# Kernel optimization log

Measured on AMD Instinct MI355X. Metric: run time of the kernel, lower is better.

The kernel has to match this reference:

```python
import jax, jax.numpy as jnp
import numpy as np

EMBED_DIM = 1024
BATCH = 4
SEQ = 2048


def setup_inputs() -> dict:
    key = jax.random.key(0)
    ks = jax.random.split(key, 9)
    D = EMBED_DIM
    s = 1.0 / np.sqrt(D)
    inputs = jax.random.normal(ks[0], (BATCH, SEQ, D), dtype=jnp.float32)
    rotation_params = jax.random.normal(ks[1], (D, D), dtype=jnp.float32) * s
    entangle_params = jax.random.normal(ks[2], (D, D), dtype=jnp.float32) * s
    Wq = jax.random.normal(ks[3], (D, D), dtype=jnp.float32) * s
    bq = jax.random.normal(ks[4], (D,), dtype=jnp.float32) * 0.01
    Wk = jax.random.normal(ks[5], (D, D), dtype=jnp.float32) * s
    bk = jax.random.normal(ks[6], (D,), dtype=jnp.float32) * 0.01
    Wv = jax.random.normal(ks[7], (D, D), dtype=jnp.float32) * s
    bv = jax.random.normal(ks[8], (D,), dtype=jnp.float32) * 0.01
    # causal mask: True = masked out (matches torch masked_fill semantics)
    mask = jnp.triu(jnp.ones((SEQ, SEQ), dtype=bool), k=1)
    return {"inputs": inputs, "rotation_params": rotation_params,
            "entangle_params": entangle_params, "Wq": Wq, "bq": bq,
            "Wk": Wk, "bk": bk, "Wv": Wv, "bv": bv, "mask": mask}


def reference(inputs, rotation_params, entangle_params, Wq, bq, Wk, bk, Wv, bv, mask):
    D = inputs.shape[-1]
    # q = Linear(x) @ R^T ; k = Linear(x) @ E^T ; v = Linear(x)
    q = (jnp.einsum('bsd,ed->bse', inputs, Wq) + bq) @ rotation_params.T
    k = (jnp.einsum('bsd,ed->bse', inputs, Wk) + bk) @ entangle_params.T
    v = jnp.einsum('bsd,ed->bse', inputs, Wv) + bv
    scores = jnp.einsum('bqd,bkd->bqk', q, k) / jnp.sqrt(jnp.float32(D))
    scores = jnp.where(mask, jnp.float32(-jnp.inf), scores)
    probs = jax.nn.softmax(scores, axis=-1)  # dropout=0.0 -> identity
    return jnp.einsum('bqk,bkd->bqd', probs, v)
```

## Files before the change

kernel.cpp:

```cpp
#include <hip/hip_runtime.h>
#include <hip/hip_bf16.h>
#include <stdint.h>
#include <math.h>

#define DD 1024
#define SS 2048
#define BB 4

typedef __bf16 bf16;
typedef __bf16 bf16x8 __attribute__((ext_vector_type(8)));
typedef __bf16 bf16x4 __attribute__((ext_vector_type(4)));
typedef float f32x4 __attribute__((ext_vector_type(4)));

__device__ __forceinline__ void gload_lds16(const bf16* g, bf16* l) {
  __builtin_amdgcn_global_load_lds(
      (const __attribute__((address_space(1))) void*)g,
      (__attribute__((address_space(3))) void*)l, 16, 0, 0);
}

__global__ __launch_bounds__(256) void prep_all(
    const float* __restrict__ x, const float* __restrict__ R,
    const float* __restrict__ E, const float* __restrict__ Wv,
    const float* __restrict__ Wq, const float* __restrict__ Wk,
    const float* __restrict__ bq, const float* __restrict__ bk,
    const float* __restrict__ bv, bf16* __restrict__ xb,
    bf16* __restrict__ Rb, bf16* __restrict__ Eb, bf16* __restrict__ Wvb,
    bf16* __restrict__ WqT, bf16* __restrict__ WkT, float* __restrict__ bias,
    float* __restrict__ rowsums) {
  int bid = blockIdx.x;
  int t = threadIdx.x;
  if (bid < 11264) {
    const float* src;
    bf16* dst;
    int base;
    if (bid < 8192) { src = x; dst = xb; base = bid; }
    else if (bid < 9216) { src = R; dst = Rb; base = bid - 8192; }
    else if (bid < 10240) { src = E; dst = Eb; base = bid - 9216; }
    else { src = Wv; dst = Wvb; base = bid - 10240; }
    int i = (base * 256 + t) * 4;
    float4 v = *(const float4*)(src + i);
    bf16x4 o;
    o.x = (bf16)v.x; o.y = (bf16)v.y; o.z = (bf16)v.z; o.w = (bf16)v.w;
    *(bf16x4*)(dst + i) = o;
  } else if (bid < 13312) {
    int r2 = bid - 11264;
    const float* src = (r2 >= 1024) ? Wk : Wq;
    bf16* dst = (r2 >= 1024) ? WkT : WqT;
    int rem = r2 & 1023;
    int bx = rem & 31, by = rem >> 5;
    __shared__ float tile[32][33];
    int tx = t & 31, ty = t >> 5;
    int xcol = bx * 32 + tx;
    int y0 = by * 32;
    for (int r = ty; r < 32; r += 8)
      tile[r][tx] = src[(y0 + r) * DD + xcol];
    __syncthreads();
    int dx = by * 32 + tx;
    int dy0 = bx * 32;
    for (int r = ty; r < 32; r += 8)
      dst[(dy0 + r) * DD + dx] = (bf16)tile[tx][r];
  } else if (bid < 16384) {
    int e = bid - 13312;
    if (e >= 2048) { if (t == 0) bias[e] = bv[e - 2048]; return; }
    const float* M = (e < 1024) ? R : E;
    const float* bb = (e < 1024) ? bq : bk;
    int row = e & 1023;
    float s = 0.f;
    for (int f = t; f < DD; f += 256) s += M[row * DD + f] * bb[f];
    for (int o = 32; o >= 1; o >>= 1) s += __shfl_xor(s, o, 64);
    __shared__ float red[4];
    if ((t & 63) == 0) red[t >> 6] = s;
    __syncthreads();
    if (t == 0) bias[e] = red[0] + red[1] + red[2] + red[3];
  } else {
    int idx = (bid - 16384) * 256 + t;
    rowsums[idx] = 0.f;
  }
}

#define QSTGA(pa, kt)                                                        \
  gload_lds16(A + (long)(w * 16 + srow) * DD + (kt) * 32 + scg,              \
              As + (pa) * 4096 + w * 512)
#define QSTGB(pb, h, kt)                                                     \
  gload_lds16(B + (long)((h) * 128 + w * 16 + srow) * DD + (kt) * 32 + scg,  \
              Bs + (pb) * 8192 + (h) * 4096 + w * 512)

#define QTILE(pa, pb, pa1, pb2, kA, kB, DOA, DOB, WAITN)                     \
  {                                                                          \
    bf16x8 af[4], bfr[4];                                                    \
    _Pragma("unroll") for (int i_ = 0; i_ < 4; i_++)                         \
        af[i_] = *(const bf16x8*)(a_base + (pa) * 4096 + i_ * 512);          \
    _Pragma("unroll") for (int j_ = 0; j_ < 4; j_++)                         \
        bfr[j_] = *(const bf16x8*)(b_base + (pb) * 8192 + j_ * 512);         \
    if (DOA) { QSTGA(pa1, kA); }                                             \
    if (DOB) { QSTGB(pb2, 0, kB); QSTGB(pb2, 1, kB); }                       \
    __builtin_amdgcn_s_barrier();                                            \
    asm volatile("s_waitcnt lgkmcnt(0)" ::: "memory");                       \
    __builtin_amdgcn_sched_barrier(0);                                       \
    __builtin_amdgcn_s_setprio(1);                                           \
    _Pragma("unroll") for (int i_ = 0; i_ < 4; i_++)                         \
        _Pragma("unroll") for (int j_ = 0; j_ < 4; j_++) acc[i_][j_] =       \
        __builtin_amdgcn_mfma_f32_16x16x32_bf16(af[i_], bfr[j_],             \
                                                acc[i_][j_], 0, 0, 0);       \
    __builtin_amdgcn_s_setprio(0);                                           \
    __builtin_amdgcn_sched_barrier(0);                                       \
    if ((WAITN) == 2) asm volatile("s_waitcnt vmcnt(2)" ::: "memory");       \
    if ((WAITN) == 0) asm volatile("s_waitcnt vmcnt(0)" ::: "memory");       \
    __builtin_amdgcn_s_barrier();                                            \
    __builtin_amdgcn_sched_barrier(0);                                       \
  }

__global__ __launch_bounds__(512, 4) void gemm_qkv(
    const bf16* __restrict__ Ag, const bf16* __restrict__ Bg,
    bf16* __restrict__ Cg, const float* __restrict__ bias,
    bf16* __restrict__ vTp) {
  __shared__ __align__(16) bf16 smem[32768];
  bf16* As = smem;
  bf16* Bs = smem + 8192;

  int id = (int)blockIdx.y * 12 + (int)blockIdx.x;
  int wg = (id & 7) * 96 + (id >> 3);
  int ck = wg / 96, r96 = wg % 96;
  int bx = (ck & 3) * 3 + r96 % 3;
  int by = (ck >> 2) * 32 + r96 / 3;
  long m0 = (long)by * 128, n0 = (long)bx * 256;
  const bf16* A = Ag + m0 * DD;
  const bf16* B = Bg + n0 * DD;

  int t = threadIdx.x;
  int w = t >> 6, l = t & 63;
  int wm = w >> 2, wn = w & 3;
  int ln = l & 15, quad = l >> 4;

  int srow = l >> 2;
  int scg = ((l & 3) ^ ((l >> 3) & 3)) * 8;
  int rdslot = (quad ^ ((ln >> 1) & 3)) * 8;
  const bf16* a_base = As + (wm * 64 + ln) * 32 + rdslot;
  const bf16* b_base = Bs + (wn * 64 + ln) * 32 + rdslot;

  f32x4 acc[4][4];
#pragma unroll
  for (int i = 0; i < 4; i++)
#pragma unroll
    for (int j = 0; j < 4; j++) acc[i][j] = f32x4{0.f, 0.f, 0.f, 0.f};

  QSTGA(0, 0);
  QSTGB(0, 0, 0); QSTGB(0, 1, 0);
  QSTGB(1, 0, 1); QSTGB(1, 1, 1);
  asm volatile("s_waitcnt vmcnt(2)" ::: "memory");
  __builtin_amdgcn_s_barrier();
  __builtin_amdgcn_sched_barrier(0);

#pragma unroll 1
  for (int t6 = 0; t6 < 30; t6 += 6) {
    QTILE(0, 0, 1, 2, t6 + 1, t6 + 2, 1, 1, 2)
    QTILE(1, 1, 0, 0, t6 + 2, t6 + 3, 1, 1, 2)
    QTILE(0, 2, 1, 1, t6 + 3, t6 + 4, 1, 1, 2)
    QTILE(1, 0, 0, 2, t6 + 4, t6 + 5, 1, 1, 2)
    QTILE(0, 1, 1, 0, t6 + 5, t6 + 6, 1, 1, 2)
    QTILE(1, 2, 0, 1, t6 + 6, t6 + 7, 1, 1, 2)
  }
  QTILE(0, 0, 1, 0, 31, 0, 1, 0, 0)
  QTILE(1, 1, 0, 0, 0, 0, 0, 0, -1)

  __syncthreads();

  if (n0 < 2048) {
    bf16* C = Cg + m0 * 3072 + n0;
#pragma unroll
    for (int i = 0; i < 4; i++) {
      int rb = wm * 64 + i * 16 + quad * 4;
#pragma unroll
      for (int j = 0; j < 4; j++) {
        int col = wn * 64 + j * 16 + ln;
        float bv_ = bias[n0 + col];
#pragma unroll
        for (int r = 0; r < 4; r++)
          C[(long)(rb + r) * 3072 + col] = (bf16)(acc[i][j][r] + bv_);
      }
    }
  } else {
    int d0 = (int)n0 - 2048;
    int b = (int)(m0 >> 11);
    int s0 = (int)(m0 & 2047);
#pragma unroll
    for (int i = 0; i < 4; i++) {
      int sl = wm * 64 + i * 16 + quad * 4;
#pragma unroll
      for (int j = 0; j < 4; j++) {
        int d = wn * 64 + j * 16 + ln;
        float bv_ = bias[n0 + d];
#pragma unroll
        for (int r = 0; r < 4; r++)
          smem[d * 128 + ((sl + r) ^ ((d & 7) << 3))] =
              (bf16)(acc[i][j][r] + bv_);
      }
    }
    __syncthreads();
    int d = t >> 1, sh = t & 1;
    bf16* dst = vTp + (long)b * DD * SS + (long)(d0 + d) * SS + s0 + sh * 64;
#pragma unroll
    for (int c = 0; c < 8; ++c) {
      int sc = (sh * 64 + c * 8) ^ ((d & 7) << 3);
      *(bf16x8*)(dst + c * 8) = *(const bf16x8*)(smem + d * 128 + sc);
    }
  }
}

template <int MODE>
__global__ __launch_bounds__(256, 4)
void gemm_bt(const bf16* __restrict__ Ag, long lda, long sAb,
             const bf16* __restrict__ Bg, long ldb, long sBb,
             void* __restrict__ Cg, long ldc, long sCb,
             const float* __restrict__ bias, float scale, int K,
             bf16* __restrict__ vTp, float* __restrict__ rowsums) {
  __shared__ __align__(16) bf16 smem[16384];
  bf16* As = smem;
  bf16* Bs = smem + 8192;

  int bx = blockIdx.x, by = blockIdx.y, bz = blockIdx.z;
  if (MODE == 0 || MODE == 1) {
    int nx = (int)gridDim.x;
    int nwg = nx * (int)gridDim.y;
    int id = by * nx + bx;
    int xcd = id & 7, rest = id >> 3;
    int q8 = nwg >> 3, r8 = nwg & 7;
    int wg = (xcd < r8 ? xcd * (q8 + 1) : r8 * (q8 + 1) + (xcd - r8) * q8)
             + rest;
    bx = wg % nx;
    by = wg / nx;
  }
  if (MODE == 1) {
    int q = bx;
    by = (int)((sqrtf(8.f * q + 1.f) - 1.f) * 0.5f);
    while ((by + 1) * (by + 2) / 2 <= q) by++;
    while (by * (by + 1) / 2 > q) by--;
    bx = q - by * (by + 1) / 2;
  }
  if (MODE == 2) by = 15 - by;
  long m0 = (long)by * 128, n0 = (long)bx * 128;
  const bf16* A = Ag + (long)bz * sAb + m0 * lda;
  const bf16* Bp = Bg + (long)bz * sBb + n0 * ldb;

  int t = threadIdx.x;
  int w = t >> 6, l = t & 63;
  int lr = l >> 2;
  int lc = (((l & 3) ^ (lr & 3)) * 8);
  int quad = l >> 4, ln = l & 15;
  int wm = w >> 1, wn = w & 1;
  int rdoff = ((quad ^ (ln & 3)) * 8);

  int Keff = (MODE == 2) ? (by + 1) * 128 : K;

  f32x4 acc[4][4];
#pragma unroll
  for (int i = 0; i < 4; i++)
#pragma unroll
    for (int j = 0; j < 4; j++) acc[i][j] = f32x4{0.f, 0.f, 0.f, 0.f};

  const bf16* a_base = As + (wm * 64 + ln) * 32 + rdoff;
  const bf16* b_base = Bs + (wn * 64 + ln) * 32 + rdoff;
  long arow0 = (long)(w * 16 + lr);

#define STG(p, kc0)                                                         \
  {                                                                         \
    int kc = (kc0) + lc;                                                    \
    gload_lds16(A + arow0 * lda + kc, As + (p) * 4096 + w * 512);           \
    gload_lds16(A + (arow0 + 64) * lda + kc,                                \
                As + (p) * 4096 + 2048 + w * 512);                          \
    gload_lds16(Bp + arow0 * ldb + kc, Bs + (p) * 4096 + w * 512);          \
    gload_lds16(Bp + (arow0 + 64) * ldb + kc,                               \
                Bs + (p) * 4096 + 2048 + w * 512);                          \
  }

  STG(0, 0);
  int cur = 0;
  for (int k = 0; k < Keff; k += 32) {
    asm volatile("s_waitcnt vmcnt(0)" ::: "memory");
    __builtin_amdgcn_s_barrier();
    __builtin_amdgcn_sched_barrier(0);
    if (k + 32 < Keff) STG(cur ^ 1, k + 32);
    bf16x8 af[4], bfr[4];
#pragma unroll
    for (int i = 0; i < 4; i++) {
      af[i] = *(const bf16x8*)(a_base + cur * 4096 + i * 512);
      bfr[i] = *(const bf16x8*)(b_base + cur * 4096 + i * 512);
    }
#pragma unroll
    for (int i = 0; i < 4; i++)
#pragma unroll
      for (int j = 0; j < 4; j++)
        acc[i][j] = __builtin_amdgcn_mfma_f32_16x16x32_bf16(
            af[i], bfr[j], acc[i][j], 0, 0, 0);
    cur ^= 1;
  }
#undef STG
  __syncthreads();

  if (MODE == 0) {
    bf16* C = (bf16*)Cg + (long)bz * sCb + m0 * ldc + n0;
#pragma unroll
    for (int i = 0; i < 4; i++) {
      int rb = wm * 64 + i * 16 + quad * 4;
#pragma unroll
      for (int j = 0; j < 4; j++) {
        int col = wn * 64 + j * 16 + ln;
        float bv_ = bias ? bias[n0 + col] : 0.f;
#pragma unroll
        for (int r = 0; r < 4; r++)
          C[(long)(rb + r) * ldc + col] = (bf16)(acc[i][j][r] + bv_);
      }
    }
  } else if (MODE == 1) {
#pragma unroll
    for (int i = 0; i < 4; i++) {
      int rb = wm * 64 + i * 16 + quad * 4;
#pragma unroll
      for (int j = 0; j < 4; j++) {
        int col = wn * 64 + j * 16 + ln;
#pragma unroll
        for (int r = 0; r < 4; r++) {
          int row = rb + r;
          float p = 0.f;
          if (n0 + col <= m0 + row) p = __expf(acc[i][j][r] * scale);
          smem[row * 128 + (col ^ ((row & 15) << 3))] = (bf16)p;
        }
      }
    }
    __syncthreads();
    int row = t >> 1, h = t & 1;
    bf16* P = (bf16*)Cg + (long)bz * sCb + (m0 + row) * ldc + n0;
    float rsum = 0.f;
#pragma unroll
    for (int jj = 0; jj < 8; jj++) {
      int p8 = h * 8 + jj;
      int slot = p8 ^ (row & 15);
      bf16x8 v = *(const bf16x8*)(smem + row * 128 + slot * 8);
#pragma unroll
      for (int e = 0; e < 8; e++) rsum += (float)v[e];
      *(bf16x8*)(P + p8 * 8) = v;
    }
    atomicAdd(&rowsums[(long)bz * SS + m0 + row], rsum);
  } else {
    float* C = (float*)Cg + (long)bz * sCb + m0 * ldc + n0;
    const float* rs = rowsums + (long)bz * SS + m0;
#pragma unroll
    for (int i = 0; i < 4; i++) {
      int rb = wm * 64 + i * 16 + quad * 4;
      float inv[4];
#pragma unroll
      for (int r = 0; r < 4; r++) inv[r] = 1.f / rs[rb + r];
#pragma unroll
      for (int j = 0; j < 4; j++) {
        int col = wn * 64 + j * 16 + ln;
#pragma unroll
        for (int r = 0; r < 4; r++)
          C[(long)(rb + r) * ldc + col] = acc[i][j][r] * inv[r];
      }
    }
  }
}

extern "C" void kernel_launch(void* const* d_in, const int* in_sizes, int n_in,
                              void* d_out, int out_size, void* d_ws,
                              size_t ws_size, hipStream_t stream) {
  const float* x = (const float*)d_in[0];
  const float* R = (const float*)d_in[1];
  const float* E = (const float*)d_in[2];
  const float* Wq = (const float*)d_in[3];
  const float* bq = (const float*)d_in[4];
  const float* Wk = (const float*)d_in[5];
  const float* bk = (const float*)d_in[6];
  const float* Wv = (const float*)d_in[7];
  const float* bv = (const float*)d_in[8];
  float* out = (float*)d_out;

  char* ws = (char*)d_ws;
  bf16* qkv = (bf16*)ws;
  bf16* vT = (bf16*)(ws + 50331648);
  bf16* probs = (bf16*)(ws + 67108864);
  float* rowsums = (float*)(ws + 100663296);
  char* sr = ws + 101711872;
  bf16* xb = (bf16*)sr;
  bf16* Rb = (bf16*)(sr + 16777216);
  bf16* Eb = Rb + 1024 * 1024;
  bf16* WqT = (bf16*)(sr + 20971520);
  bf16* WkT = WqT + 1024 * 1024;
  bf16* wcat = (bf16*)(sr + 25165824);
  float* bias = (float*)(sr + 31457280);

  prep_all<<<16416, 256, 0, stream>>>(x, R, E, Wv, Wq, Wk, bq, bk, bv, xb, Rb,
                                      Eb, wcat + 2048 * DD, WqT, WkT, bias,
                                      rowsums);

  gemm_bt<0><<<dim3(8, 8, 2), 256, 0, stream>>>(
      Rb, DD, 1024 * 1024, WqT, DD, 1024 * 1024, wcat, DD, 1024 * 1024,
      nullptr, 1.f, DD, nullptr, nullptr);

  gemm_qkv<<<dim3(12, 64, 1), 512, 0, stream>>>(xb, wcat, qkv, bias, vT);

  gemm_bt<1><<<dim3(136, 1, BB), 256, 0, stream>>>(
      qkv, 3072, (long)SS * 3072, qkv + 1024, 3072, (long)SS * 3072, probs,
      SS, (long)SS * SS, nullptr, 0.03125f, DD, nullptr, rowsums);

  gemm_bt<2><<<dim3(8, 16, BB), 256, 0, stream>>>(
      probs, SS, (long)SS * SS, vT, SS, (long)DD * SS, out,
      DD, (long)SS * DD, nullptr, 1.f, SS, nullptr, rowsums);
}
```

Baseline: 293.2 us.

## Replace causal scores GEMM with 128x256-tile, 512-thread pipelined kernel

The QK^T scores stage moves out of the generic 128x128 gemm_bt MODE 1 path into a dedicated scores256 kernel. It reuses the gemm_qkv triple-buffered LDS pipeline with 512 threads and 128x256 tiles, and enumerates only causal tiles through a square-root mapping combined with XCD-aware ordering. Its epilogue applies exp and the causal mask, writes P through swizzled LDS, and reduces row sums with shuffles before the atomic add. The larger tiles should give more data reuse per block and fewer launched blocks, at the cost of more wasted work on diagonal tiles and possible load imbalance.

```diff
diff --git a/kernel.cpp b/kernel.cpp
--- a/kernel.cpp
+++ b/kernel.cpp
@@ -110,6 +110,24 @@
     __builtin_amdgcn_sched_barrier(0);                                       \
   }
 
+#define QPROLOGUE_AND_LOOP                                                   \
+  QSTGA(0, 0);                                                               \
+  QSTGB(0, 0, 0); QSTGB(0, 1, 0);                                            \
+  QSTGB(1, 0, 1); QSTGB(1, 1, 1);                                            \
+  asm volatile("s_waitcnt vmcnt(2)" ::: "memory");                           \
+  __builtin_amdgcn_s_barrier();                                              \
+  __builtin_amdgcn_sched_barrier(0);                                         \
+  _Pragma("unroll 1") for (int t6 = 0; t6 < 30; t6 += 6) {                   \
+    QTILE(0, 0, 1, 2, t6 + 1, t6 + 2, 1, 1, 2)                               \
+    QTILE(1, 1, 0, 0, t6 + 2, t6 + 3, 1, 1, 2)                               \
+    QTILE(0, 2, 1, 1, t6 + 3, t6 + 4, 1, 1, 2)                               \
+    QTILE(1, 0, 0, 2, t6 + 4, t6 + 5, 1, 1, 2)                               \
+    QTILE(0, 1, 1, 0, t6 + 5, t6 + 6, 1, 1, 2)                               \
+    QTILE(1, 2, 0, 1, t6 + 6, t6 + 7, 1, 1, 2)                               \
+  }                                                                          \
+  QTILE(0, 0, 1, 0, 31, 0, 1, 0, 0)     \
+  QTILE(1, 1, 0, 0, 0, 0, 0, 0, -1)
+
 __global__ __launch_bounds__(512, 4) void gemm_qkv(
     const bf16* __restrict__ Ag, const bf16* __restrict__ Bg,
     bf16* __restrict__ Cg, const float* __restrict__ bias,
@@ -144,24 +162,7 @@
 #pragma unroll
     for (int j = 0; j < 4; j++) acc[i][j] = f32x4{0.f, 0.f, 0.f, 0.f};
 
-  QSTGA(0, 0);
-  QSTGB(0, 0, 0); QSTGB(0, 1, 0);
-  QSTGB(1, 0, 1); QSTGB(1, 1, 1);
-  asm volatile("s_waitcnt vmcnt(2)" ::: "memory");
-  __builtin_amdgcn_s_barrier();
-  __builtin_amdgcn_sched_barrier(0);
-
-#pragma unroll 1
-  for (int t6 = 0; t6 < 30; t6 += 6) {
-    QTILE(0, 0, 1, 2, t6 + 1, t6 + 2, 1, 1, 2)
-    QTILE(1, 1, 0, 0, t6 + 2, t6 + 3, 1, 1, 2)
-    QTILE(0, 2, 1, 1, t6 + 3, t6 + 4, 1, 1, 2)
-    QTILE(1, 0, 0, 2, t6 + 4, t6 + 5, 1, 1, 2)
-    QTILE(0, 1, 1, 0, t6 + 5, t6 + 6, 1, 1, 2)
-    QTILE(1, 2, 0, 1, t6 + 6, t6 + 7, 1, 1, 2)
-  }
-  QTILE(0, 0, 1, 0, 31, 0, 1, 0, 0)
-  QTILE(1, 1, 0, 0, 0, 0, 0, 0, -1)
+  QPROLOGUE_AND_LOOP
 
   __syncthreads();
 
@@ -205,6 +206,129 @@
       *(bf16x8*)(dst + c * 8) = *(const bf16x8*)(smem + d * 128 + sc);
     }
   }
+}
+
+#define CSTGA(pa, kt)                                                        \
+  gload_lds16(Aq + (long)(w * 16 + srow) * 3072 + (kt) * 32 + scg,           \
+              As + (pa) * 4096 + w * 512)
+#define CSTGB(pb, h, kt)                                                     \
+  gload_lds16(Bk + (long)((h) * 128 + w * 16 + srow) * 3072 + (kt) * 32 +    \
+                  scg,                                                       \
+              Bs + (pb) * 8192 + (h) * 4096 + w * 512)
+
+#define CTILE(pa, pb, pa1, pb2, kA, kB, DOA, DOB, WAITN)                     \
+  {                                                                          \
+    bf16x8 af[4], bfr[4];                                                    \
+    _Pragma("unroll") for (int i_ = 0; i_ < 4; i_++)                         \
+        af[i_] = *(const bf16x8*)(a_base + (pa) * 4096 + i_ * 512);          \
+    _Pragma("unroll") for (int j_ = 0; j_ < 4; j_++)                         \
+        bfr[j_] = *(const bf16x8*)(b_base + (pb) * 8192 + j_ * 512);         \
+    if (DOA) { CSTGA(pa1, kA); }                                             \
+    if (DOB) { CSTGB(pb2, 0, kB); CSTGB(pb2, 1, kB); }                       \
+    __builtin_amdgcn_s_barrier();                                            \
+    asm volatile("s_waitcnt lgkmcnt(0)" ::: "memory");                       \
+    __builtin_amdgcn_sched_barrier(0);                                       \
+    __builtin_amdgcn_s_setprio(1);                                           \
+    _Pragma("unroll") for (int i_ = 0; i_ < 4; i_++)                         \
+        _Pragma("unroll") for (int j_ = 0; j_ < 4; j_++) acc[i_][j_] =       \
+        __builtin_amdgcn_mfma_f32_16x16x32_bf16(af[i_], bfr[j_],             \
+                                                acc[i_][j_], 0, 0, 0);       \
+    __builtin_amdgcn_s_setprio(0);                                           \
+    __builtin_amdgcn_sched_barrier(0);                                       \
+    if ((WAITN) == 2) asm volatile("s_waitcnt vmcnt(2)" ::: "memory");       \
+    if ((WAITN) == 0) asm volatile("s_waitcnt vmcnt(0)" ::: "memory");       \
+    __builtin_amdgcn_s_barrier();                                            \
+    __builtin_amdgcn_sched_barrier(0);                                       \
+  }
+
+__global__ __launch_bounds__(512, 4) void scores256(
+    const bf16* __restrict__ qkvp, bf16* __restrict__ P,
+    float* __restrict__ rowsums) {
+  __shared__ __align__(16) bf16 smem[32768];
+  bf16* As = smem;
+  bf16* Bs = smem + 8192;
+
+  int bz = blockIdx.z;
+  int id = (int)blockIdx.x;
+  int q = (id & 7) * 9 + (id >> 3);
+  int s = (int)sqrtf((float)q + 0.5f);
+  while (s * s > q) s--;
+  while ((s + 1) * (s + 1) <= q) s++;
+  int by, bxc;
+  if (q >= s * (s + 1)) { by = 2 * s; bxc = q - s * (s + 1); }
+  else { by = 2 * s - 1; bxc = q - s * s; }
+  long m0 = (long)by * 128, n0 = (long)bxc * 256;
+  const bf16* Aq = qkvp + (long)bz * SS * 3072 + m0 * 3072;
+  const bf16* Bk = qkvp + 1024 + (long)bz * SS * 3072 + n0 * 3072;
+
+  int t = threadIdx.x;
+  int w = t >> 6, l = t & 63;
+  int wm = w >> 2, wn = w & 3;
+  int ln = l & 15, quad = l >> 4;
+
+  int srow = l >> 2;
+  int scg = ((l & 3) ^ ((l >> 3) & 3)) * 8;
+  int rdslot = (quad ^ ((ln >> 1) & 3)) * 8;
+  const bf16* a_base = As + (wm * 64 + ln) * 32 + rdslot;
+  const bf16* b_base = Bs + (wn * 64 + ln) * 32 + rdslot;
+
+  f32x4 acc[4][4];
+#pragma unroll
+  for (int i = 0; i < 4; i++)
+#pragma unroll
+    for (int j = 0; j < 4; j++) acc[i][j] = f32x4{0.f, 0.f, 0.f, 0.f};
+
+  CSTGA(0, 0);
+  CSTGB(0, 0, 0); CSTGB(0, 1, 0);
+  CSTGB(1, 0, 1); CSTGB(1, 1, 1);
+  asm volatile("s_waitcnt vmcnt(2)" ::: "memory");
+  __builtin_amdgcn_s_barrier();
+  __builtin_amdgcn_sched_barrier(0);
+#pragma unroll 1
+  for (int t6 = 0; t6 < 30; t6 += 6) {
+    CTILE(0, 0, 1, 2, t6 + 1, t6 + 2, 1, 1, 2)
+    CTILE(1, 1, 0, 0, t6 + 2, t6 + 3, 1, 1, 2)
+    CTILE(0, 2, 1, 1, t6 + 3, t6 + 4, 1, 1, 2)
+    CTILE(1, 0, 0, 2, t6 + 4, t6 + 5, 1, 1, 2)
+    CTILE(0, 1, 1, 0, t6 + 5, t6 + 6, 1, 1, 2)
+    CTILE(1, 2, 0, 1, t6 + 6, t6 + 7, 1, 1, 2)
+  }
+  CTILE(0, 0, 1, 0, 31, 0, 1, 0, 0)
+  CTILE(1, 1, 0, 0, 0, 0, 0, 0, -1)
+
+  __syncthreads();
+
+#pragma unroll
+  for (int i = 0; i < 4; i++) {
+    int rb = wm * 64 + i * 16 + quad * 4;
+#pragma unroll
+    for (int j = 0; j < 4; j++) {
+      int col = wn * 64 + j * 16 + ln;
+#pragma unroll
+      for (int r = 0; r < 4; r++) {
+        int row = rb + r;
+        float p = 0.f;
+        if (n0 + col <= m0 + row) p = __expf(acc[i][j][r] * 0.03125f);
+        smem[row * 256 + (col ^ ((row & 7) << 3))] = (bf16)p;
+      }
+    }
+  }
+  __syncthreads();
+  int row = t >> 2, qtr = t & 3;
+  bf16* Pr = P + (long)bz * SS * SS + (m0 + row) * SS + n0;
+  float rsum = 0.f;
+#pragma unroll
+  for (int c8 = 0; c8 < 8; c8++) {
+    int p8 = qtr * 8 + c8;
+    int slot = p8 ^ (row & 7);
+    bf16x8 v = *(const bf16x8*)(smem + row * 256 + slot * 8);
+#pragma unroll
+    for (int e = 0; e < 8; e++) rsum += (float)v[e];
+    *(bf16x8*)(Pr + p8 * 8) = v;
+  }
+  rsum += __shfl_xor(rsum, 1, 64);
+  rsum += __shfl_xor(rsum, 2, 64);
+  if (qtr == 0) atomicAdd(&rowsums[(long)bz * SS + m0 + row], rsum);
 }
 
 template <int MODE>
@@ -219,7 +343,7 @@
   bf16* Bs = smem + 8192;
 
   int bx = blockIdx.x, by = blockIdx.y, bz = blockIdx.z;
-  if (MODE == 0 || MODE == 1) {
+  if (MODE == 0) {
     int nx = (int)gridDim.x;
     int nwg = nx * (int)gridDim.y;
     int id = by * nx + bx;
@@ -230,13 +354,6 @@
     bx = wg % nx;
     by = wg / nx;
   }
-  if (MODE == 1) {
-    int q = bx;
-    by = (int)((sqrtf(8.f * q + 1.f) - 1.f) * 0.5f);
-    while ((by + 1) * (by + 2) / 2 <= q) by++;
-    while (by * (by + 1) / 2 > q) by--;
-    bx = q - by * (by + 1) / 2;
-  }
   if (MODE == 2) by = 15 - by;
   long m0 = (long)by * 128, n0 = (long)bx * 128;
   const bf16* A = Ag + (long)bz * sAb + m0 * lda;
@@ -311,36 +428,6 @@
           C[(long)(rb + r) * ldc + col] = (bf16)(acc[i][j][r] + bv_);
       }
     }
-  } else if (MODE == 1) {
-#pragma unroll
-    for (int i = 0; i < 4; i++) {
-      int rb = wm * 64 + i * 16 + quad * 4;
-#pragma unroll
-      for (int j = 0; j < 4; j++) {
-        int col = wn * 64 + j * 16 + ln;
-#pragma unroll
-        for (int r = 0; r < 4; r++) {
-          int row = rb + r;
-          float p = 0.f;
-          if (n0 + col <= m0 + row) p = __expf(acc[i][j][r] * scale);
-          smem[row * 128 + (col ^ ((row & 15) << 3))] = (bf16)p;
-        }
-      }
-    }
-    __syncthreads();
-    int row = t >> 1, h = t & 1;
-    bf16* P = (bf16*)Cg + (long)bz * sCb + (m0 + row) * ldc + n0;
-    float rsum = 0.f;
-#pragma unroll
-    for (int jj = 0; jj < 8; jj++) {
-      int p8 = h * 8 + jj;
-      int slot = p8 ^ (row & 15);
-      bf16x8 v = *(const bf16x8*)(smem + row * 128 + slot * 8);
-#pragma unroll
-      for (int e = 0; e < 8; e++) rsum += (float)v[e];
-      *(bf16x8*)(P + p8 * 8) = v;
-    }
-    atomicAdd(&rowsums[(long)bz * SS + m0 + row], rsum);
   } else {
     float* C = (float*)Cg + (long)bz * sCb + m0 * ldc + n0;
     const float* rs = rowsums + (long)bz * SS + m0;
@@ -399,9 +486,7 @@
 
   gemm_qkv<<<dim3(12, 64, 1), 512, 0, stream>>>(xb, wcat, qkv, bias, vT);
 
-  gemm_bt<1><<<dim3(136, 1, BB), 256, 0, stream>>>(
-      qkv, 3072, (long)SS * 3072, qkv + 1024, 3072, (long)SS * 3072, probs,
-      SS, (long)SS * SS, nullptr, 0.03125f, DD, nullptr, rowsums);
+  scores256<<<dim3(72, 1, BB), 512, 0, stream>>>(qkv, probs, rowsums);
 
   gemm_bt<2><<<dim3(8, 16, BB), 256, 0, stream>>>(
       probs, SS, (long)SS * SS, vT, SS, (long)DD * SS, out,
```

New measurement: 290.6 us. No clear change (-0.9%).
